# Kernel optimization log

Measured on AMD Instinct MI355X. Metric: run time of the kernel, lower is better.

Reference implementation:

```python
import jax, jax.numpy as jnp
import numpy as np

CHUNK = 64


def _rmsnorm(x, g, eps=1e-6):
    return x * jax.lax.rsqrt(jnp.mean(x * x, axis=-1, keepdims=True) + eps) * g


def setup_inputs() -> dict:
    key = jax.random.key(0)
    ks = jax.random.split(key, 8)
    B, L, D, N = 4, 4096, 512, 64
    s = 0.02
    return {
        'x': jax.random.normal(ks[0], (B, L, D), jnp.float32),
        'A_log': -jnp.ones((D,), jnp.float32) * jnp.log(2.0),
        'dt_bias': jnp.log(jnp.expm1(jax.random.uniform(ks[1], (D,), jnp.float32, 0.001, 0.1))),
        'D_skip': jnp.ones((D,), jnp.float32),
        'W_xproj': jax.random.normal(ks[2], (D, 2 * D), jnp.float32) * s,
        'b_xproj': jnp.zeros((2 * D,), jnp.float32),
        'W_B': jax.random.normal(ks[3], (D, N), jnp.float32) * s,
        'W_C': jax.random.normal(ks[4], (D, N), jnp.float32) * s,
        'W_dt': jax.random.normal(ks[5], (D, D), jnp.float32) * s,
        'g_Bnorm': jnp.ones((N,), jnp.float32),
        'g_Cnorm': jnp.ones((N,), jnp.float32),
        'g_outnorm': jnp.ones((D,), jnp.float32),
        'W_out': jax.random.normal(ks[6], (D, D), jnp.float32) * s,
        'b_out': jnp.zeros((D,), jnp.float32),
    }


def reference(x, A_log, dt_bias, D_skip, W_xproj, b_xproj, W_B, W_C, W_dt,
              g_Bnorm, g_Cnorm, g_outnorm, W_out, b_out):
    b, l, d = x.shape
    n = W_B.shape[1]
    p = CHUNK
    c = l // p  # L chosen divisible by chunk size (original pads otherwise)

    A = -jnp.exp(jnp.clip(A_log, -20.0, 2.0))  # (d,)
    xp = x @ W_xproj + b_xproj                  # (b,l,2d)
    x_bar, z = jnp.split(xp, 2, axis=-1)
    Bm = _rmsnorm(x_bar @ W_B, g_Bnorm)         # (b,l,n)
    Cm = _rmsnorm(x_bar @ W_C, g_Cnorm)         # (b,l,n)
    dt = jnp.clip(jax.nn.softplus(x_bar @ W_dt + dt_bias), 1e-4, 5.0)
    A_bar = jnp.exp(jnp.clip(dt * A, -20.0, 0.0))  # (b,l,d)

    to_chunks = lambda t: t.reshape(b, c, p, t.shape[-1]).transpose(1, 0, 2, 3)
    xc, Bc, Cc, Ac = map(to_chunks, (x_bar, Bm, Cm, A_bar))  # (c,b,p,*)
    mask = jnp.tril(jnp.ones((p, p), x.dtype))

    def process_chunk(prev_state, inputs):
        x_c, B_c, C_c, A_c = inputs
        log_a = jnp.log(jnp.clip(A_c, 1e-8, 1.0))
        la_cs = jnp.cumsum(log_a, axis=1)  # (b,p,d)
        # intra-chunk decay matrix M: (b,p,p,d)
        M = jnp.exp(la_cs[:, :, None, :] - la_cs[:, None, :, :]) * mask[None, :, :, None]
        BX = jnp.einsum('bpn,bpd->bpnd', B_c, x_c)
        state = jnp.einsum('bijd,bjnd->bind', M, BX)
        y_intra = jnp.einsum('bpn,bpnd->bpd', C_c, state)
        decay = jnp.exp(la_cs)
        y_inter = jnp.einsum('bpn,bpnd->bpd', C_c,
                             prev_state[:, None, :, :] * decay[:, :, None, :])
        y_c = y_intra + y_inter
        a_total = jnp.exp(la_cs[:, -1, :])             # (b,d)
        a_to_end = jnp.exp(la_cs[:, -1:, :] - la_cs)   # (b,p,d)
        chunk_state = jnp.einsum('bpn,bpd->bnd', B_c, x_c * a_to_end)
        new_state = prev_state * a_total[:, None, :] + chunk_state
        new_state = jnp.where(jnp.isfinite(new_state), new_state, 0.0)
        y_c = jnp.where(jnp.isfinite(y_c), y_c, 0.0)
        return new_state, y_c

    init = jnp.zeros((b, n, d), x.dtype)
    _, yc = jax.lax.scan(jax.checkpoint(process_chunk), init, (xc, Bc, Cc, Ac))
    y = yc.transpose(1, 0, 2, 3).reshape(b, l, d)
    y = jnp.where(jnp.isfinite(y), y, 0.0)
    y = y + D_skip * x_bar
    y = _rmsnorm(y, g_outnorm) * jax.nn.silu(z)
    return y @ W_out + b_out
```

## Files before the change

kernel.cpp:

```cpp
#include <hip/hip_runtime.h>
#include <hip/hip_bf16.h>
#include <math.h>

typedef __hip_bfloat16 bf16;
typedef __attribute__((ext_vector_type(8))) short short8;
typedef __attribute__((ext_vector_type(4))) float floatx4;

#define B_ 4
#define L_ 4096
#define D_ 512
#define M_ (B_*L_)

__device__ __forceinline__ float b2f(bf16 v){ return __bfloat162float(v); }
__device__ __forceinline__ bf16  f2b(float v){ return __float2bfloat16(v); }
__device__ __forceinline__ short f2bs(float v){ bf16 h = __float2bfloat16(v); short s; __builtin_memcpy(&s,&h,2); return s; }
__device__ __forceinline__ unsigned short f2bus(float v){ bf16 h = __float2bfloat16(v); unsigned short s; __builtin_memcpy(&s,&h,2); return s; }
__device__ __forceinline__ float bus2f(unsigned short u){ unsigned int x = ((unsigned int)u)<<16; float f; __builtin_memcpy(&f,&x,4); return f; }
__device__ __forceinline__ floatx4 fx4(float v){ floatx4 r; r.x=v; r.y=v; r.z=v; r.w=v; return r; }
__device__ __forceinline__ floatx4 us4f(ushort4 u){ floatx4 r; r.x=bus2f(u.x); r.y=bus2f(u.y); r.z=bus2f(u.z); r.w=bus2f(u.w); return r; }
__device__ __forceinline__ ushort4 f4us(floatx4 v){ ushort4 r; r.x=f2bus(v.x); r.y=f2bus(v.y); r.z=f2bus(v.z); r.w=f2bus(v.w); return r; }
__device__ __forceinline__ floatx4 exp4(floatx4 v){ floatx4 r; r.x=__expf(v.x); r.y=__expf(v.y); r.z=__expf(v.z); r.w=__expf(v.w); return r; }

#define GLD16(gp, lp) __builtin_amdgcn_global_load_lds( \
    (const __attribute__((address_space(1))) void*)(gp), \
    (__attribute__((address_space(3))) void*)(lp), 16, 0, 0)

__global__ __launch_bounds__(1024) void k_transpose(const float* __restrict__ src,
                                                    bf16* __restrict__ dst, int K, int N){
    __shared__ float tile[32][33];
    int n0 = blockIdx.x*32, k0 = blockIdx.y*32;
    int tx = threadIdx.x, ty = threadIdx.y;
    tile[ty][tx] = src[(size_t)(k0+ty)*N + n0+tx];
    __syncthreads();
    ((short*)dst)[(size_t)(n0+ty)*K + k0+tx] = f2bs(tile[tx][ty]);
}

__global__ __launch_bounds__(256) void k_cvt(const float* __restrict__ src,
                                             bf16* __restrict__ dst){
    size_t i = ((size_t)blockIdx.x*256 + threadIdx.x)*4;
    float4 v = *(const float4*)(src + i);
    short4 s; s.x=f2bs(v.x); s.y=f2bs(v.y); s.z=f2bs(v.z); s.w=f2bs(v.w);
    *(short4*)((short*)dst + i) = s;
}

template<int EPI>
__global__ __launch_bounds__(256) void k_gemm(const bf16* __restrict__ Ap,
        const bf16* __restrict__ Wt, const float* __restrict__ bias,
        const float* __restrict__ aux,
        float* __restrict__ o1, bf16* __restrict__ o2, bf16* __restrict__ o3,
        float* __restrict__ o4){
    __shared__ short As[128*32];
    __shared__ short Bs[128*32];
    const int K = 512;
    int m0 = blockIdx.x*128, n0 = blockIdx.y*128;
    int tid=threadIdx.x, w=tid>>6, lane=tid&63;
    int wr=w>>1, wc=w&1, quad=lane>>4, r16=lane&15;
    floatx4 acc[4][4];
    #pragma unroll
    for (int i=0;i<4;i++)
        #pragma unroll
        for (int j=0;j<4;j++)
            #pragma unroll
            for (int e=0;e<4;e++) acc[i][j][e]=0.f;

    int c0 = tid, c1 = tid + 256;
    const short* Ab = (const short*)Ap + (size_t)m0*K;
    const short* Wb = (const short*)Wt + (size_t)n0*K;
    int r0 = c0>>2, g0 = (c0&3)*8;
    int r1 = c1>>2, g1 = (c1&3)*8;

    for (int k0=0;k0<K;k0+=32){
        GLD16(Ab + (size_t)r0*K + k0 + g0, &As[c0*8]);
        GLD16(Ab + (size_t)r1*K + k0 + g1, &As[c1*8]);
        GLD16(Wb + (size_t)r0*K + k0 + g0, &Bs[c0*8]);
        GLD16(Wb + (size_t)r1*K + k0 + g1, &Bs[c1*8]);
        __syncthreads();
        short8 af[4], bv[4];
        #pragma unroll
        for (int i=0;i<4;i++) af[i] = *(short8*)&As[(wr*64+i*16+r16)*32 + quad*8];
        #pragma unroll
        for (int j=0;j<4;j++) bv[j] = *(short8*)&Bs[(wc*64+j*16+r16)*32 + quad*8];
        #pragma unroll
        for (int i=0;i<4;i++)
            #pragma unroll
            for (int j=0;j<4;j++)
                acc[i][j] = __builtin_amdgcn_mfma_f32_16x16x32_bf16(af[i], bv[j], acc[i][j], 0,0,0);
        __syncthreads();
    }
    if (EPI==3){
        #pragma unroll
        for (int i=0;i<4;i++)
        #pragma unroll
        for (int reg=0;reg<4;reg++){
            float ss=0.f;
            #pragma unroll
            for (int j=0;j<4;j++){ float t=acc[i][j][reg]; ss+=t*t; }
            #pragma unroll
            for (int m=1;m<16;m<<=1) ss += __shfl_xor(ss, m, 64);
            float rq = rsqrtf(ss*(1.f/64.f)+1e-6f);
            int gr = m0 + wr*64 + i*16 + quad*4 + reg;
            #pragma unroll
            for (int j=0;j<4;j++){
                int gc = wc*64 + j*16 + r16;
                float gval = (gc<64) ? bias[gc] : aux[gc-64];
                float v = acc[i][j][reg]*rq*gval;
                if (gc<64) o1[(size_t)gr*64 + gc] = v;
                else       o4[(size_t)gr*64 + (gc-64)] = v;
            }
        }
        return;
    }
    #pragma unroll
    for (int i=0;i<4;i++)
    #pragma unroll
    for (int j=0;j<4;j++)
    #pragma unroll
    for (int reg=0;reg<4;reg++){
        int gr = m0 + wr*64 + i*16 + quad*4 + reg;
        int gc = n0 + wc*64 + j*16 + r16;
        float v = acc[i][j][reg] + bias[gc];
        if (EPI==0){
            if (gc < 512){
                o2[(size_t)gr*512 + gc] = f2b(v);
            } else {
                o3[(size_t)gr*512 + (gc-512)] = f2b(v / (1.f + __expf(-v)));
            }
        } else if (EPI==1){
            float sp = (v > 15.f) ? v : log1pf(__expf(v));
            float dt = fminf(fmaxf(sp, 1e-4f), 5.f);
            float Ad = -__expf(fminf(fmaxf(aux[gc], -20.f), 2.f));
            o2[(size_t)gr*512 + gc] = f2b(fminf(fmaxf(dt*Ad, -18.420680743952367f), 0.f));
        } else {
            o1[(size_t)gr*512 + gc] = v;
        }
    }
}

__global__ __launch_bounds__(128) void k_pass1(const unsigned short* __restrict__ lah,
        const unsigned short* __restrict__ xh, const float* __restrict__ Bm,
        unsigned short* __restrict__ localh, float* __restrict__ atot){
    __shared__ float Bs[64*32];
    int c=blockIdx.x, b=blockIdx.y, nh=blockIdx.z;
    int d = threadIdx.x*4;
    size_t rowbase=(size_t)b*L_+(size_t)c*64;
    size_t cb=(size_t)c*4+b;
    #pragma unroll
    for (int it=0;it<4;it++){
        int idx=it*128+threadIdx.x;
        int row=idx>>3, grp=idx&7;
        *(float4*)&Bs[row*32+grp*4] = *(const float4*)(Bm + (rowbase+row)*64 + nh*32 + grp*4);
    }
    __syncthreads();
    floatx4 st[32];
    #pragma unroll
    for (int n=0;n<32;n++) st[n]=fx4(0.f);
    floatx4 cs=fx4(0.f);
    size_t off0=rowbase*512+d;
    #pragma unroll 1
    for (int i=0;i<64;i++){
        floatx4 lai = us4f(*(const ushort4*)(lah+off0+(size_t)i*512));
        floatx4 xi  = us4f(*(const ushort4*)(xh +off0+(size_t)i*512));
        floatx4 ai = exp4(lai);
        cs = cs + lai;
        const float* Br=Bs+i*32;
        #pragma unroll
        for (int k=0;k<8;k++){
            float4 bv=*(const float4*)(Br+k*4);
            st[k*4+0]=ai*st[k*4+0]+fx4(bv.x)*xi;
            st[k*4+1]=ai*st[k*4+1]+fx4(bv.y)*xi;
            st[k*4+2]=ai*st[k*4+2]+fx4(bv.z)*xi;
            st[k*4+3]=ai*st[k*4+3]+fx4(bv.w)*xi;
        }
    }
    #pragma unroll
    for (int n=0;n<32;n++)
        *(ushort4*)(localh + (cb*64 + nh*32 + n)*512 + d) = f4us(st[n]);
    if (nh==0){
        floatx4 at = exp4(cs);
        *(floatx4*)(atot + cb*512 + d) = at;
    }
}

__global__ __launch_bounds__(256) void k_scan(unsigned short* __restrict__ localh,
        const float* __restrict__ atot){
    int idx = blockIdx.x*256 + threadIdx.x;
    int d = (idx & 255)*2, n = (idx >> 8) & 63, b = idx >> 14;
    float sx=0.f, sy=0.f;
    for (int c=0;c<64;c++){
        size_t cb = (size_t)c*4 + b;
        size_t off = (cb*64 + n)*512 + d;
        ushort2 v = *(ushort2*)(localh+off);
        float vx=bus2f(v.x), vy=bus2f(v.y);
        ushort2 wp; wp.x=f2bus(sx); wp.y=f2bus(sy);
        *(ushort2*)(localh+off) = wp;
        float2 at = *(const float2*)(atot + cb*512 + d);
        sx = sx*at.x + vx; sy = sy*at.y + vy;
        if (!isfinite(sx)) sx = 0.f;
        if (!isfinite(sy)) sy = 0.f;
    }
}

__global__ __launch_bounds__(128) void k_pass2(const unsigned short* __restrict__ lah,
        const unsigned short* __restrict__ xh, const float* __restrict__ Bm,
        const float* __restrict__ Cm, const unsigned short* __restrict__ Sprevh,
        unsigned short* __restrict__ ybuf){
    __shared__ float Bs[64*32];
    __shared__ float Cs[64*32];
    int c=blockIdx.x, b=blockIdx.y, nh=blockIdx.z;
    int d = threadIdx.x*4;
    size_t rowbase=(size_t)b*L_+(size_t)c*64;
    size_t cb=(size_t)c*4+b;
    #pragma unroll
    for (int it=0;it<4;it++){
        int idx=it*128+threadIdx.x;
        int row=idx>>3, grp=idx&7;
        *(float4*)&Bs[row*32+grp*4] = *(const float4*)(Bm + (rowbase+row)*64 + nh*32 + grp*4);
        *(float4*)&Cs[row*32+grp*4] = *(const float4*)(Cm + (rowbase+row)*64 + nh*32 + grp*4);
    }
    floatx4 st[32];
    #pragma unroll
    for (int n=0;n<32;n++)
        st[n] = us4f(*(const ushort4*)(Sprevh + (cb*64 + nh*32 + n)*512 + d));
    __syncthreads();
    size_t off0=rowbase*512+d;
    unsigned short* yout = ybuf + (size_t)nh*M_*512;
    #pragma unroll 1
    for (int i=0;i<64;i++){
        floatx4 lai = us4f(*(const ushort4*)(lah+off0+(size_t)i*512));
        floatx4 xi  = us4f(*(const ushort4*)(xh +off0+(size_t)i*512));
        floatx4 ai = exp4(lai);
        const float* Br=Bs+i*32;
        const float* Cr=Cs+i*32;
        floatx4 yv=fx4(0.f);
        #pragma unroll
        for (int k=0;k<8;k++){
            float4 bv=*(const float4*)(Br+k*4);
            float4 cv=*(const float4*)(Cr+k*4);
            floatx4 s;
            s=ai*st[k*4+0]+fx4(bv.x)*xi; st[k*4+0]=s; yv=yv+fx4(cv.x)*s;
            s=ai*st[k*4+1]+fx4(bv.y)*xi; st[k*4+1]=s; yv=yv+fx4(cv.y)*s;
            s=ai*st[k*4+2]+fx4(bv.z)*xi; st[k*4+2]=s; yv=yv+fx4(cv.z)*s;
            s=ai*st[k*4+3]+fx4(bv.w)*xi; st[k*4+3]=s; yv=yv+fx4(cv.w)*s;
        }
        *(ushort4*)(yout + off0 + (size_t)i*512) = f4us(yv);
    }
}

__global__ __launch_bounds__(256) void k_outnorm(const unsigned short* __restrict__ yA,
        const unsigned short* __restrict__ yB,
        const bf16* __restrict__ xbarh, const float* __restrict__ Dskip,
        const float* __restrict__ g, const bf16* __restrict__ siluz,
        bf16* __restrict__ u){
    int wave = threadIdx.x >> 6, lane = threadIdx.x & 63;
    size_t row = (size_t)blockIdx.x*4 + wave;
    float v[8]; float ss = 0.f;
    #pragma unroll
    for (int j=0;j<8;j++){
        int d = j*64 + lane;
        float yv = bus2f(yA[row*512 + d]) + bus2f(yB[row*512 + d]);
        if (!isfinite(yv)) yv = 0.f;
        float t = yv + Dskip[d] * b2f(xbarh[row*512 + d]);
        v[j] = t; ss += t*t;
    }
    #pragma unroll
    for (int m=1;m<64;m<<=1) ss += __shfl_xor(ss, m, 64);
    float r = rsqrtf(ss*(1.f/512.f) + 1e-6f);
    #pragma unroll
    for (int j=0;j<8;j++){
        int d = j*64 + lane;
        u[row*512 + d] = f2b(v[j] * r * g[d] * b2f(siluz[row*512 + d]));
    }
}

extern "C" void kernel_launch(void* const* d_in, const int* in_sizes, int n_in,
                              void* d_out, int out_size, void* d_ws, size_t ws_size,
                              hipStream_t stream){
    const float* x       = (const float*)d_in[0];
    const float* A_log   = (const float*)d_in[1];
    const float* dt_bias = (const float*)d_in[2];
    const float* D_skip  = (const float*)d_in[3];
    const float* W_xproj = (const float*)d_in[4];
    const float* b_xproj = (const float*)d_in[5];
    const float* W_B     = (const float*)d_in[6];
    const float* W_C     = (const float*)d_in[7];
    const float* W_dt    = (const float*)d_in[8];
    const float* g_B     = (const float*)d_in[9];
    const float* g_C     = (const float*)d_in[10];
    const float* g_out   = (const float*)d_in[11];
    const float* W_out   = (const float*)d_in[12];
    const float* b_out   = (const float*)d_in[13];
    float* out = (float*)d_out;

    char* wp = (char*)d_ws;
    auto alloc = [&](size_t bytes)->char*{ char* p = wp; wp += (bytes + 255) & ~(size_t)255; return p; };
    bf16*  xh    = (bf16*) alloc((size_t)M_*512*2);
    bf16*  xbarh = (bf16*) alloc((size_t)M_*512*2);
    bf16*  siluz = (bf16*) alloc((size_t)M_*512*2);
    bf16*  lah   = (bf16*) alloc((size_t)M_*512*2);
    float* Bm    = (float*)alloc((size_t)M_*64*4);
    float* Cm    = (float*)alloc((size_t)M_*64*4);
    unsigned short* localh = (unsigned short*)alloc((size_t)256*64*512*2);
    float* atot  = (float*)alloc((size_t)256*512*4);
    unsigned short* ybuf = (unsigned short*)alloc((size_t)2*M_*512*2);
    bf16*  u     = (bf16*) alloc((size_t)M_*512*2);
    bf16*  WtX   = (bf16*) alloc((size_t)1024*512*2);
    bf16*  WtD   = (bf16*) alloc((size_t)512*512*2);
    bf16*  WtO   = (bf16*) alloc((size_t)512*512*2);
    bf16*  WtBC  = (bf16*) alloc((size_t)128*512*2);

    dim3 tb(32,32);
    k_transpose<<<dim3(32,16), tb, 0, stream>>>(W_xproj, WtX, 512, 1024);
    k_transpose<<<dim3(16,16), tb, 0, stream>>>(W_dt,   WtD, 512, 512);
    k_transpose<<<dim3(16,16), tb, 0, stream>>>(W_out,  WtO, 512, 512);
    k_transpose<<<dim3(2,16),  tb, 0, stream>>>(W_B,    WtBC,          512, 64);
    k_transpose<<<dim3(2,16),  tb, 0, stream>>>(W_C,    WtBC+64*512,   512, 64);
    k_cvt      <<<M_*512/1024, 256, 0, stream>>>(x, xh);

    k_gemm<0> <<<dim3(128, 8), 256, 0, stream>>>(xh,    WtX,  b_xproj, nullptr, nullptr, xbarh, siluz, nullptr);
    k_gemm<3> <<<dim3(128, 1), 256, 0, stream>>>(xbarh, WtBC, g_B, g_C, Bm, nullptr, nullptr, Cm);
    k_gemm<1> <<<dim3(128, 4), 256, 0, stream>>>(xbarh, WtD,  dt_bias, A_log, nullptr, lah, nullptr, nullptr);
    k_pass1   <<<dim3(64,4,2), 128, 0, stream>>>((const unsigned short*)lah, (const unsigned short*)xbarh, Bm, localh, atot);
    k_scan    <<<256,          256, 0, stream>>>(localh, atot);
    k_pass2   <<<dim3(64,4,2), 128, 0, stream>>>((const unsigned short*)lah, (const unsigned short*)xbarh, Bm, Cm, localh, ybuf);
    k_outnorm <<<M_/4,         256, 0, stream>>>(ybuf, ybuf+(size_t)M_*512, xbarh, D_skip, g_out, siluz, u);
    k_gemm<2> <<<dim3(128, 4), 256, 0, stream>>>(u,     WtO,  b_out, nullptr, out, nullptr, nullptr, nullptr);
}
```

Baseline: 382.1 us.

## Merge prep launches and software-pipeline chunk scan loads in pass kernels

Five weight transposes and the x conversion are merged into one kernel launch to cut launch overhead. In k_pass1 and k_pass2 the per-row loop is unrolled by two and double-buffers the global la/x loads and the shared B/C row reads, so the next row's loads are issued before the current row's FMA chain. This is meant to hide memory latency in the sequential recurrence loop. The price is more register pressure from the 32-entry state plus the prefetched B and C buffers at 128 threads, which could cause spills or lower occupancy.

```diff
diff --git a/kernel.cpp b/kernel.cpp
--- a/kernel.cpp
+++ b/kernel.cpp
@@ -25,22 +25,32 @@
     (const __attribute__((address_space(1))) void*)(gp), \
     (__attribute__((address_space(3))) void*)(lp), 16, 0, 0)
 
-__global__ __launch_bounds__(1024) void k_transpose(const float* __restrict__ src,
-                                                    bf16* __restrict__ dst, int K, int N){
+__global__ __launch_bounds__(1024) void k_prep(const float* __restrict__ x, bf16* __restrict__ xh,
+        const float* __restrict__ WX, const float* __restrict__ WD, const float* __restrict__ WO,
+        const float* __restrict__ WB, const float* __restrict__ WC,
+        bf16* __restrict__ WtX, bf16* __restrict__ WtD, bf16* __restrict__ WtO,
+        bf16* __restrict__ WtBC){
     __shared__ float tile[32][33];
-    int n0 = blockIdx.x*32, k0 = blockIdx.y*32;
-    int tx = threadIdx.x, ty = threadIdx.y;
-    tile[ty][tx] = src[(size_t)(k0+ty)*N + n0+tx];
-    __syncthreads();
-    ((short*)dst)[(size_t)(n0+ty)*K + k0+tx] = f2bs(tile[tx][ty]);
-}
-
-__global__ __launch_bounds__(256) void k_cvt(const float* __restrict__ src,
-                                             bf16* __restrict__ dst){
-    size_t i = ((size_t)blockIdx.x*256 + threadIdx.x)*4;
-    float4 v = *(const float4*)(src + i);
-    short4 s; s.x=f2bs(v.x); s.y=f2bs(v.y); s.z=f2bs(v.z); s.w=f2bs(v.w);
-    *(short4*)((short*)dst + i) = s;
+    int bx = blockIdx.x;
+    if (bx < 1088){
+        const float* src; bf16* dst; int N, t;
+        if (bx < 512)      { src=WX; dst=WtX;  N=1024; t=bx; }
+        else if (bx < 768) { src=WD; dst=WtD;  N=512;  t=bx-512; }
+        else if (bx < 1024){ src=WO; dst=WtO;  N=512;  t=bx-768; }
+        else if (bx < 1056){ src=WB; dst=WtBC; N=64;   t=bx-1024; }
+        else               { src=WC; dst=WtBC+(size_t)64*512; N=64; t=bx-1056; }
+        int ntiles = N >> 5;
+        int n0 = (t & (ntiles-1))*32, k0 = (t/ntiles)*32;
+        int tx = threadIdx.x & 31, ty = threadIdx.x >> 5;
+        tile[ty][tx] = src[(size_t)(k0+ty)*N + n0+tx];
+        __syncthreads();
+        ((short*)dst)[(size_t)(n0+ty)*512 + k0+tx] = f2bs(tile[tx][ty]);
+    } else {
+        size_t i = ((size_t)(bx-1088)*1024 + threadIdx.x)*4;
+        float4 v = *(const float4*)(x + i);
+        short4 s; s.x=f2bs(v.x); s.y=f2bs(v.y); s.z=f2bs(v.z); s.w=f2bs(v.w);
+        *(short4*)((short*)xh + i) = s;
+    }
 }
 
 template<int EPI>
@@ -136,10 +146,24 @@
     }
 }
 
+template<bool YACC>
+__device__ __forceinline__ void row_step(floatx4* st, const float4* Bb, const float4* Cb,
+        floatx4 ai, floatx4 xi, floatx4& yv){
+    #pragma unroll
+    for (int k=0;k<8;k++){
+        float4 bv=Bb[k];
+        floatx4 s;
+        s=ai*st[k*4+0]+fx4(bv.x)*xi; st[k*4+0]=s; if (YACC) yv=yv+fx4(Cb[k].x)*s;
+        s=ai*st[k*4+1]+fx4(bv.y)*xi; st[k*4+1]=s; if (YACC) yv=yv+fx4(Cb[k].y)*s;
+        s=ai*st[k*4+2]+fx4(bv.z)*xi; st[k*4+2]=s; if (YACC) yv=yv+fx4(Cb[k].z)*s;
+        s=ai*st[k*4+3]+fx4(bv.w)*xi; st[k*4+3]=s; if (YACC) yv=yv+fx4(Cb[k].w)*s;
+    }
+}
+
 __global__ __launch_bounds__(128) void k_pass1(const unsigned short* __restrict__ lah,
         const unsigned short* __restrict__ xh, const float* __restrict__ Bm,
         unsigned short* __restrict__ localh, float* __restrict__ atot){
-    __shared__ float Bs[64*32];
+    __shared__ float Bsh[64*32];
     int c=blockIdx.x, b=blockIdx.y, nh=blockIdx.z;
     int d = threadIdx.x*4;
     size_t rowbase=(size_t)b*L_+(size_t)c*64;
@@ -148,7 +172,7 @@
     for (int it=0;it<4;it++){
         int idx=it*128+threadIdx.x;
         int row=idx>>3, grp=idx&7;
-        *(float4*)&Bs[row*32+grp*4] = *(const float4*)(Bm + (rowbase+row)*64 + nh*32 + grp*4);
+        *(float4*)&Bsh[row*32+grp*4] = *(const float4*)(Bm + (rowbase+row)*64 + nh*32 + grp*4);
     }
     __syncthreads();
     floatx4 st[32];
@@ -156,29 +180,34 @@
     for (int n=0;n<32;n++) st[n]=fx4(0.f);
     floatx4 cs=fx4(0.f);
     size_t off0=rowbase*512+d;
-    #pragma unroll 1
-    for (int i=0;i<64;i++){
-        floatx4 lai = us4f(*(const ushort4*)(lah+off0+(size_t)i*512));
-        floatx4 xi  = us4f(*(const ushort4*)(xh +off0+(size_t)i*512));
-        floatx4 ai = exp4(lai);
-        cs = cs + lai;
-        const float* Br=Bs+i*32;
-        #pragma unroll
-        for (int k=0;k<8;k++){
-            float4 bv=*(const float4*)(Br+k*4);
-            st[k*4+0]=ai*st[k*4+0]+fx4(bv.x)*xi;
-            st[k*4+1]=ai*st[k*4+1]+fx4(bv.y)*xi;
-            st[k*4+2]=ai*st[k*4+2]+fx4(bv.z)*xi;
-            st[k*4+3]=ai*st[k*4+3]+fx4(bv.w)*xi;
-        }
+    ushort4 laA=*(const ushort4*)(lah+off0),     xA=*(const ushort4*)(xh+off0);
+    ushort4 laB=*(const ushort4*)(lah+off0+512), xB=*(const ushort4*)(xh+off0+512);
+    float4 Ab[8], Bb[8];
+    #pragma unroll
+    for (int k=0;k<8;k++) Ab[k]=*(const float4*)&Bsh[k*4];
+    floatx4 dummy;
+    for (int i=0;i<64;i+=2){
+        int r2 = (i+2<64)? i+2 : 63;
+        int r3 = (i+3<64)? i+3 : 63;
+        floatx4 la1=us4f(laA), x1=us4f(xA);
+        laA=*(const ushort4*)(lah+off0+(size_t)r2*512); xA=*(const ushort4*)(xh+off0+(size_t)r2*512);
+        #pragma unroll
+        for (int k=0;k<8;k++) Bb[k]=*(const float4*)&Bsh[(i+1)*32+k*4];
+        cs = cs + la1;
+        row_step<false>(st, Ab, nullptr, exp4(la1), x1, dummy);
+
+        floatx4 la2=us4f(laB), x2=us4f(xB);
+        laB=*(const ushort4*)(lah+off0+(size_t)r3*512); xB=*(const ushort4*)(xh+off0+(size_t)r3*512);
+        #pragma unroll
+        for (int k=0;k<8;k++) Ab[k]=*(const float4*)&Bsh[r2*32+k*4];
+        cs = cs + la2;
+        row_step<false>(st, Bb, nullptr, exp4(la2), x2, dummy);
     }
     #pragma unroll
     for (int n=0;n<32;n++)
         *(ushort4*)(localh + (cb*64 + nh*32 + n)*512 + d) = f4us(st[n]);
-    if (nh==0){
-        floatx4 at = exp4(cs);
-        *(floatx4*)(atot + cb*512 + d) = at;
-    }
+    if (nh==0)
+        *(floatx4*)(atot + cb*512 + d) = exp4(cs);
 }
 
 __global__ __launch_bounds__(256) void k_scan(unsigned short* __restrict__ localh,
@@ -204,8 +233,8 @@
         const unsigned short* __restrict__ xh, const float* __restrict__ Bm,
         const float* __restrict__ Cm, const unsigned short* __restrict__ Sprevh,
         unsigned short* __restrict__ ybuf){
-    __shared__ float Bs[64*32];
-    __shared__ float Cs[64*32];
+    __shared__ float Bsh[64*32];
+    __shared__ float Csh[64*32];
     int c=blockIdx.x, b=blockIdx.y, nh=blockIdx.z;
     int d = threadIdx.x*4;
     size_t rowbase=(size_t)b*L_+(size_t)c*64;
@@ -214,8 +243,8 @@
     for (int it=0;it<4;it++){
         int idx=it*128+threadIdx.x;
         int row=idx>>3, grp=idx&7;
-        *(float4*)&Bs[row*32+grp*4] = *(const float4*)(Bm + (rowbase+row)*64 + nh*32 + grp*4);
-        *(float4*)&Cs[row*32+grp*4] = *(const float4*)(Cm + (rowbase+row)*64 + nh*32 + grp*4);
+        *(float4*)&Bsh[row*32+grp*4] = *(const float4*)(Bm + (rowbase+row)*64 + nh*32 + grp*4);
+        *(float4*)&Csh[row*32+grp*4] = *(const float4*)(Cm + (rowbase+row)*64 + nh*32 + grp*4);
     }
     floatx4 st[32];
     #pragma unroll
@@ -224,25 +253,29 @@
     __syncthreads();
     size_t off0=rowbase*512+d;
     unsigned short* yout = ybuf + (size_t)nh*M_*512;
-    #pragma unroll 1
-    for (int i=0;i<64;i++){
-        floatx4 lai = us4f(*(const ushort4*)(lah+off0+(size_t)i*512));
-        floatx4 xi  = us4f(*(const ushort4*)(xh +off0+(size_t)i*512));
-        floatx4 ai = exp4(lai);
-        const float* Br=Bs+i*32;
-        const float* Cr=Cs+i*32;
+    ushort4 laA=*(const ushort4*)(lah+off0),     xA=*(const ushort4*)(xh+off0);
+    ushort4 laB=*(const ushort4*)(lah+off0+512), xB=*(const ushort4*)(xh+off0+512);
+    float4 Ab[8], Ac[8], Bb[8], Bc[8];
+    #pragma unroll
+    for (int k=0;k<8;k++){ Ab[k]=*(const float4*)&Bsh[k*4]; Ac[k]=*(const float4*)&Csh[k*4]; }
+    for (int i=0;i<64;i+=2){
+        int r2 = (i+2<64)? i+2 : 63;
+        int r3 = (i+3<64)? i+3 : 63;
+        floatx4 la1=us4f(laA), x1=us4f(xA);
+        laA=*(const ushort4*)(lah+off0+(size_t)r2*512); xA=*(const ushort4*)(xh+off0+(size_t)r2*512);
+        #pragma unroll
+        for (int k=0;k<8;k++){ Bb[k]=*(const float4*)&Bsh[(i+1)*32+k*4]; Bc[k]=*(const float4*)&Csh[(i+1)*32+k*4]; }
         floatx4 yv=fx4(0.f);
-        #pragma unroll
-        for (int k=0;k<8;k++){
-            float4 bv=*(const float4*)(Br+k*4);
-            float4 cv=*(const float4*)(Cr+k*4);
-            floatx4 s;
-            s=ai*st[k*4+0]+fx4(bv.x)*xi; st[k*4+0]=s; yv=yv+fx4(cv.x)*s;
-            s=ai*st[k*4+1]+fx4(bv.y)*xi; st[k*4+1]=s; yv=yv+fx4(cv.y)*s;
-            s=ai*st[k*4+2]+fx4(bv.z)*xi; st[k*4+2]=s; yv=yv+fx4(cv.z)*s;
-            s=ai*st[k*4+3]+fx4(bv.w)*xi; st[k*4+3]=s; yv=yv+fx4(cv.w)*s;
-        }
-        *(ushort4*)(yout + off0 + (size_t)i*512) = f4us(yv);
+        row_step<true>(st, Ab, Ac, exp4(la1), x1, yv);
+        *(ushort4*)(yout+off0+(size_t)i*512)=f4us(yv);
+
+        floatx4 la2=us4f(laB), x2=us4f(xB);
+        laB=*(const ushort4*)(lah+off0+(size_t)r3*512); xB=*(const ushort4*)(xh+off0+(size_t)r3*512);
+        #pragma unroll
+        for (int k=0;k<8;k++){ Ab[k]=*(const float4*)&Bsh[r2*32+k*4]; Ac[k]=*(const float4*)&Csh[r2*32+k*4]; }
+        floatx4 yv2=fx4(0.f);
+        row_step<true>(st, Bb, Bc, exp4(la2), x2, yv2);
+        *(ushort4*)(yout+off0+(size_t)(i+1)*512)=f4us(yv2);
     }
 }
 
@@ -308,14 +341,8 @@
     bf16*  WtO   = (bf16*) alloc((size_t)512*512*2);
     bf16*  WtBC  = (bf16*) alloc((size_t)128*512*2);
 
-    dim3 tb(32,32);
-    k_transpose<<<dim3(32,16), tb, 0, stream>>>(W_xproj, WtX, 512, 1024);
-    k_transpose<<<dim3(16,16), tb, 0, stream>>>(W_dt,   WtD, 512, 512);
-    k_transpose<<<dim3(16,16), tb, 0, stream>>>(W_out,  WtO, 512, 512);
-    k_transpose<<<dim3(2,16),  tb, 0, stream>>>(W_B,    WtBC,          512, 64);
-    k_transpose<<<dim3(2,16),  tb, 0, stream>>>(W_C,    WtBC+64*512,   512, 64);
-    k_cvt      <<<M_*512/1024, 256, 0, stream>>>(x, xh);
-
+    k_prep    <<<3136, 1024, 0, stream>>>(x, xh, W_xproj, W_dt, W_out, W_B, W_C,
+                                          WtX, WtD, WtO, WtBC);
     k_gemm<0> <<<dim3(128, 8), 256, 0, stream>>>(xh,    WtX,  b_xproj, nullptr, nullptr, xbarh, siluz, nullptr);
     k_gemm<3> <<<dim3(128, 1), 256, 0, stream>>>(xbarh, WtBC, g_B, g_C, Bm, nullptr, nullptr, Cm);
     k_gemm<1> <<<dim3(128, 4), 256, 0, stream>>>(xbarh, WtD,  dt_bias, A_log, nullptr, lah, nullptr, nullptr);
```

Result: faster. 353.4 us (-7.5%).
